# Kernel tuning notes

Hardware: AMD Instinct MI355X
Metric: run time of the kernel (lower is better)

Reference implementation:

```python
import jax, jax.numpy as jnp
import numpy as np

EMBED = 1024
HEADS = 16
HEAD_DIM = EMBED // HEADS


def setup_inputs() -> dict:
    key = jax.random.key(0)
    ks = jax.random.split(key, 7)
    N, S = 2, 2048
    k = jax.random.normal(ks[0], (N, S, EMBED), dtype=jnp.float32)
    q = jax.random.normal(ks[1], (N, S, EMBED), dtype=jnp.float32)
    v = jax.random.normal(ks[2], (N, S, EMBED), dtype=jnp.float32)
    sc = 1.0 / np.sqrt(HEAD_DIM)
    # nn.Linear weights, applied as x @ W.T
    Wk = jax.random.normal(ks[3], (HEAD_DIM, HEAD_DIM), dtype=jnp.float32) * sc
    Wq = jax.random.normal(ks[4], (HEAD_DIM, HEAD_DIM), dtype=jnp.float32) * sc
    Wv = jax.random.normal(ks[5], (HEAD_DIM, HEAD_DIM), dtype=jnp.float32) * sc
    Wo = jax.random.normal(ks[6], (EMBED, EMBED), dtype=jnp.float32) / np.sqrt(EMBED)
    return {"k": k, "q": q, "v": v, "Wk": Wk, "Wq": Wq, "Wv": Wv, "Wo": Wo}


def reference(k, q, v, Wk, Wq, Wv, Wo):
    N, S, _ = q.shape
    # reshape to [N, S, H, D]; per-head projection weights shared across heads
    kh = jnp.einsum('nshd,ed->nshe', k.reshape(N, S, HEADS, HEAD_DIM), Wk)
    qh = jnp.einsum('nshd,ed->nshe', q.reshape(N, S, HEADS, HEAD_DIM), Wq)
    vh = jnp.einsum('nshd,ed->nshe', v.reshape(N, S, HEADS, HEAD_DIM), Wv)
    # energy: [N, H, q_len, k_len]
    energy = jnp.einsum('nqhd,nkhd->nhqk', qh, kh)
    attn = jax.nn.softmax(energy / jnp.sqrt(jnp.float32(HEAD_DIM)), axis=-1)
    out = jnp.einsum('nhqk,nkhd->nqhd', attn, vh).reshape(N, S, EMBED)
    return out @ Wo.T
```

## Files before the change

kernel.cpp:

```cpp
#include <hip/hip_runtime.h>

#define SQ   2048
#define HEADS 16
#define HD   64
#define EMB  1024

typedef __attribute__((ext_vector_type(2))) __fp16 h2;
typedef __attribute__((ext_vector_type(4))) __fp16 h4;
typedef __attribute__((ext_vector_type(8))) __fp16 h8;
typedef __attribute__((ext_vector_type(4))) float f4;
typedef unsigned short USH;
typedef unsigned int   UI;

__device__ __forceinline__ UI pkh(float a, float b) {
    h2 v = __builtin_amdgcn_cvt_pkrtz(a, b);
    return __builtin_bit_cast(UI, v);
}

__device__ __forceinline__ void glds16(const void* g, void* l) {
    __builtin_amdgcn_global_load_lds(
        (const __attribute__((address_space(1))) unsigned int*)g,
        (__attribute__((address_space(3))) unsigned int*)l, 16, 0, 0);
}

__global__ __launch_bounds__(256) void proj_fused(
    const float* __restrict__ q_in, const float* __restrict__ k_in,
    const float* __restrict__ v_in, const float* __restrict__ Wq,
    const float* __restrict__ Wk,   const float* __restrict__ Wv,
    const float* __restrict__ Wo,
    USH* __restrict__ Qh, USH* __restrict__ Kh, USH* __restrict__ Vt,
    USH* __restrict__ Wob)
{
    int t = threadIdx.x;
    if (blockIdx.y == 3) {
        int i = blockIdx.x * 256 + t;
        for (int j = 0; j < 4; ++j) {
            float4 v = ((const float4*)Wo)[i + j * 65536];
            uint2 pk; pk.x = pkh(v.x, v.y); pk.y = pkh(v.z, v.w);
            *(uint2*)(Wob + ((size_t)i + (size_t)j * 65536) * 4) = pk;
        }
        return;
    }
    const float* X = (blockIdx.y == 0) ? q_in : (blockIdx.y == 1) ? k_in : v_in;
    const float* W = (blockIdx.y == 0) ? Wq   : (blockIdx.y == 1) ? Wk   : Wv;
    float scale    = (blockIdx.y == 0) ? 0.18033688011112043f : 1.0f;

    int bx = (blockIdx.x & 7) * 32 + (blockIdx.x >> 3);

    __shared__ __align__(16) USH Xl[256][72];
    __shared__ __align__(16) USH Wl[64][72];

    const float4* Xg = (const float4*)(X + (size_t)bx * 16384);
    for (int j = 0; j < 16; ++j) {
        int f = t + j * 256;
        float4 v = Xg[f];
        int row = f >> 4; int col = (f & 15) << 2;
        uint2 pk; pk.x = pkh(v.x, v.y); pk.y = pkh(v.z, v.w);
        *(uint2*)&Xl[row][col] = pk;
    }
    const float4* Wg = (const float4*)W;
    for (int j = 0; j < 4; ++j) {
        int f = t + j * 256;
        float4 v = Wg[f];
        int row = f >> 4; int col = (f & 15) << 2;
        uint2 pk; pk.x = pkh(v.x, v.y); pk.y = pkh(v.z, v.w);
        *(uint2*)&Wl[row][col] = pk;
    }
    __syncthreads();

    int wv = t >> 6, lane = t & 63, l4 = lane & 15, quad = lane >> 4;

    h8 wf[4][2], xf[4][2];
    for (int et = 0; et < 4; ++et)
        for (int ks = 0; ks < 2; ++ks)
            wf[et][ks] = *(const h8*)&Wl[et * 16 + l4][ks * 32 + quad * 8];
    for (int rt = 0; rt < 4; ++rt)
        for (int ks = 0; ks < 2; ++ks)
            xf[rt][ks] = *(const h8*)&Xl[wv * 64 + rt * 16 + l4][ks * 32 + quad * 8];

    f4 acc[4][4];
    for (int et = 0; et < 4; ++et)
        for (int rt = 0; rt < 4; ++rt) acc[et][rt] = (f4)(0.0f);
    for (int et = 0; et < 4; ++et)
        for (int rt = 0; rt < 4; ++rt)
            for (int ks = 0; ks < 2; ++ks)
                acc[et][rt] = __builtin_amdgcn_mfma_f32_16x16x32_f16(
                    wf[et][ks], xf[rt][ks], acc[et][rt], 0, 0, 0);

    if (blockIdx.y == 2) {
        int ns0 = bx * 16 + wv * 4;
        int n = ns0 >> 11, s = ns0 & 2047;
        for (int et = 0; et < 4; ++et)
            for (int j = 0; j < 4; ++j) {
                int e = et * 16 + quad * 4 + j;
                uint2 pk;
                pk.x = pkh(acc[et][0][j], acc[et][1][j]);
                pk.y = pkh(acc[et][2][j], acc[et][3][j]);
                *(uint2*)(Vt + (((size_t)(n * HEADS + l4) * HD + e) * SQ + s)) = pk;
            }
    } else {
        USH* Out = (blockIdx.y == 0) ? Qh : Kh;
        for (int rt = 0; rt < 4; ++rt) {
            int ns = bx * 16 + wv * 4 + rt;
            int n = ns >> 11, s = ns & 2047;
            USH* ob = Out + (((size_t)(n * HEADS) + l4) * SQ + s) * HD;
            for (int et = 0; et < 4; ++et) {
                uint2 pk;
                pk.x = pkh(acc[et][rt][0] * scale, acc[et][rt][1] * scale);
                pk.y = pkh(acc[et][rt][2] * scale, acc[et][rt][3] * scale);
                *(uint2*)(ob + et * 16 + quad * 4) = pk;
            }
        }
    }
}

__device__ __forceinline__ void stage_stripe(const USH* __restrict__ Kg,
                                             const USH* __restrict__ Vg,
                                             int kt, USH* wbuf,
                                             int w, int lane)
{
#pragma unroll
    for (int j = 0; j < 2; ++j) {
        int chunk = (lane >> 4) + j * 4;
        glds16(Kg + (size_t)(kt * 64 + w * 16 + (lane & 15)) * HD + chunk * 8,
               wbuf + j * 512);
    }
#pragma unroll
    for (int j = 0; j < 2; ++j) {
        int d = ((lane >> 5) + j * 2) * 16 + ((lane & 31) >> 1);
        glds16(Vg + (size_t)d * SQ + kt * 64 + w * 16 + (lane & 1) * 8,
               wbuf + 1024 + j * 512);
    }
}

__global__ __launch_bounds__(256, 3) void attn_kernel(
    const USH* __restrict__ Qh, const USH* __restrict__ Kh,
    const USH* __restrict__ Vt, USH* __restrict__ Oh)
{
    __shared__ union {
        USH wbuf[4][3][2048];
        struct { float Osum[64][68]; float Lsum[64]; } r;
    } lds;

    int t = threadIdx.x, w = t >> 6, lane = t & 63;
    int l4 = lane & 15, quad = lane >> 4;
    int b = blockIdx.x;
    int nh = b & 31;
    int q0 = (b >> 5) * 64;
    const USH* Qg = Qh + ((size_t)nh * SQ + q0) * HD;
    const USH* Kg = Kh + (size_t)nh * SQ * HD;
    const USH* Vg = Vt + (size_t)nh * HD * SQ;

    h8 bq[4][2];
#pragma unroll
    for (int qt = 0; qt < 4; ++qt)
#pragma unroll
        for (int ks = 0; ks < 2; ++ks)
            bq[qt][ks] = *(const h8*)(Qg + (size_t)(qt * 16 + l4) * HD + ks * 32 + quad * 8);

    f4 o[4][4];
#pragma unroll
    for (int dt = 0; dt < 4; ++dt)
#pragma unroll
        for (int qt = 0; qt < 4; ++qt) o[dt][qt] = (f4)(0.0f);
    float lsum[4] = {0.f, 0.f, 0.f, 0.f};

    int koff = quad * 128 + l4 * 8;
    int voff = 1024 + l4 * 16 + quad * 4;

    stage_stripe(Kg, Vg, 0, lds.wbuf[w][0], w, lane);
    stage_stripe(Kg, Vg, 1, lds.wbuf[w][1], w, lane);

    for (int i = 0; i < 16; ++i) {
        int tA = 2 * i, tB = 2 * i + 1;
        USH* bufA = lds.wbuf[w][tA % 3];
        USH* bufB = lds.wbuf[w][tB % 3];

        asm volatile("s_waitcnt vmcnt(0)" ::: "memory");
        __builtin_amdgcn_sched_barrier(0);

        h8 akA0 = *(const h8*)(bufA + koff);
        h8 akA1 = *(const h8*)(bufA + 512 + koff);
        h8 akB0 = *(const h8*)(bufB + koff);
        h8 akB1 = *(const h8*)(bufB + 512 + koff);
        h8 av8[4];
#pragma unroll
        for (int dt = 0; dt < 4; ++dt) {
            uint2 lo = *(const uint2*)(bufA + voff + dt * 256);
            uint2 hi = *(const uint2*)(bufB + voff + dt * 256);
            uint4 u; u.x = lo.x; u.y = lo.y; u.z = hi.x; u.w = hi.y;
            av8[dt] = __builtin_bit_cast(h8, u);
        }
        asm volatile("s_waitcnt lgkmcnt(0)" ::: "memory");
        __builtin_amdgcn_sched_barrier(0);
        if (i < 15) {
            stage_stripe(Kg, Vg, tA + 2, lds.wbuf[w][(tA + 2) % 3], w, lane);
            stage_stripe(Kg, Vg, tB + 2, lds.wbuf[w][(tB + 2) % 3], w, lane);
        }

        uint2 pA[4];
#pragma unroll
        for (int qt = 0; qt < 4; ++qt) {
            f4 s0 = __builtin_amdgcn_mfma_f32_16x16x32_f16(akA0, bq[qt][0], (f4)(0.0f), 0, 0, 0);
            f4 sc = __builtin_amdgcn_mfma_f32_16x16x32_f16(akA1, bq[qt][1], s0, 0, 0, 0);
            float p0 = __builtin_amdgcn_exp2f(sc[0]);
            float p1 = __builtin_amdgcn_exp2f(sc[1]);
            float p2 = __builtin_amdgcn_exp2f(sc[2]);
            float p3 = __builtin_amdgcn_exp2f(sc[3]);
            lsum[qt] += (p0 + p1) + (p2 + p3);
            pA[qt].x = pkh(p0, p1); pA[qt].y = pkh(p2, p3);
        }

#pragma unroll
        for (int qt = 0; qt < 4; ++qt) {
            f4 s0 = __builtin_amdgcn_mfma_f32_16x16x32_f16(akB0, bq[qt][0], (f4)(0.0f), 0, 0, 0);
            f4 sc = __builtin_amdgcn_mfma_f32_16x16x32_f16(akB1, bq[qt][1], s0, 0, 0, 0);
            float p0 = __builtin_amdgcn_exp2f(sc[0]);
            float p1 = __builtin_amdgcn_exp2f(sc[1]);
            float p2 = __builtin_amdgcn_exp2f(sc[2]);
            float p3 = __builtin_amdgcn_exp2f(sc[3]);
            lsum[qt] += (p0 + p1) + (p2 + p3);
            uint4 u;
            u.x = pA[qt].x; u.y = pA[qt].y;
            u.z = pkh(p0, p1); u.w = pkh(p2, p3);
            h8 pp = __builtin_bit_cast(h8, u);
#pragma unroll
            for (int dt = 0; dt < 4; ++dt)
                o[dt][qt] = __builtin_amdgcn_mfma_f32_16x16x32_f16(
                    av8[dt], pp, o[dt][qt], 0, 0, 0);
        }
    }

#pragma unroll
    for (int qt = 0; qt < 4; ++qt) {
        lsum[qt] += __shfl_xor(lsum[qt], 16, 64);
        lsum[qt] += __shfl_xor(lsum[qt], 32, 64);
    }

    __syncthreads();
    for (int ph = 0; ph < 4; ++ph) {
        if (w == ph) {
            for (int dt = 0; dt < 4; ++dt)
                for (int qt = 0; qt < 4; ++qt) {
                    float* dst = &lds.r.Osum[qt * 16 + l4][dt * 16 + quad * 4];
                    f4 val = o[dt][qt];
                    if (ph) val += *(const f4*)dst;
                    *(f4*)dst = val;
                }
            if (quad == 0)
                for (int qt = 0; qt < 4; ++qt) {
                    int qi = qt * 16 + l4;
                    lds.r.Lsum[qi] = ph ? (lds.r.Lsum[qi] + lsum[qt]) : lsum[qt];
                }
        }
        __syncthreads();
    }

    int n = nh >> 4, h = nh & 15;
    int q = t >> 2, d0 = (t & 3) * 16;
    float inv = 1.0f / lds.r.Lsum[q];
    float vv[16];
#pragma unroll
    for (int i = 0; i < 4; ++i) {
        f4 x = *(const f4*)&lds.r.Osum[q][d0 + i * 4];
        vv[i * 4 + 0] = x[0] * inv; vv[i * 4 + 1] = x[1] * inv;
        vv[i * 4 + 2] = x[2] * inv; vv[i * 4 + 3] = x[3] * inv;
    }
    uint4 ou0, ou1;
    ou0.x = pkh(vv[0], vv[1]);   ou0.y = pkh(vv[2], vv[3]);
    ou0.z = pkh(vv[4], vv[5]);   ou0.w = pkh(vv[6], vv[7]);
    ou1.x = pkh(vv[8], vv[9]);   ou1.y = pkh(vv[10], vv[11]);
    ou1.z = pkh(vv[12], vv[13]); ou1.w = pkh(vv[14], vv[15]);
    USH* ob = Oh + ((size_t)(n * SQ + q0 + q)) * EMB + h * HD + d0;
    *(uint4*)ob = ou0;
    *(uint4*)(ob + 8) = ou1;
}

__global__ __launch_bounds__(256, 4) void gemm_bt(const USH* __restrict__ A,
                                                  const USH* __restrict__ B,
                                                  float* __restrict__ C)
{
    __shared__ __align__(16) USH Al[2][4096];
    __shared__ __align__(16) USH Bl[2][4096];
    int t = threadIdx.x, w = t >> 6, lane = t & 63;
    int l4 = lane & 15, quad = lane >> 4;
    int b = blockIdx.x;
    int m0 = (b & 63) * 64;
    int n0 = (b >> 6) * 64;
    int wm = (w >> 1) * 32, wn = (w & 1) * 32;

    f4 acc[2][2];
    for (int mt = 0; mt < 2; ++mt)
        for (int nt = 0; nt < 2; ++nt) acc[mt][nt] = (f4)(0.0f);

    int aslot[2][2], bslot[2][2];
#pragma unroll
    for (int mt = 0; mt < 2; ++mt)
#pragma unroll
        for (int ks = 0; ks < 2; ++ks) {
            int m = wm + mt * 16 + l4;
            aslot[mt][ks] = m * 8 + ((ks * 4 + quad) ^ (m & 7));
            int nn = wn + mt * 16 + l4;
            bslot[mt][ks] = nn * 8 + ((ks * 4 + quad) ^ (nn & 7));
        }

#pragma unroll
    for (int j = 0; j < 2; ++j) {
        int s = (w * 2 + j) * 64 + lane;
        int r = s >> 3, c = (s & 7) ^ (r & 7);
        glds16(A + (size_t)(m0 + r) * 1024 + c * 8, Al[0] + s * 8);
        glds16(B + (size_t)(n0 + r) * 1024 + c * 8, Bl[0] + s * 8);
    }

    for (int ki = 0; ki < 16; ++ki) {
        int cur = ki & 1;
        __syncthreads();
        if (ki + 1 < 16) {
            int k0 = (ki + 1) * 64;
#pragma unroll
            for (int j = 0; j < 2; ++j) {
                int s = (w * 2 + j) * 64 + lane;
                int r = s >> 3, c = (s & 7) ^ (r & 7);
                glds16(A + (size_t)(m0 + r) * 1024 + k0 + c * 8, Al[cur ^ 1] + s * 8);
                glds16(B + (size_t)(n0 + r) * 1024 + k0 + c * 8, Bl[cur ^ 1] + s * 8);
            }
        }

        h8 a[2][2], bf[2][2];
#pragma unroll
        for (int mt = 0; mt < 2; ++mt)
#pragma unroll
            for (int ks = 0; ks < 2; ++ks) {
                a[mt][ks]  = *(const h8*)(Al[cur] + aslot[mt][ks] * 8);
                bf[mt][ks] = *(const h8*)(Bl[cur] + bslot[mt][ks] * 8);
            }
#pragma unroll
        for (int mt = 0; mt < 2; ++mt)
#pragma unroll
            for (int nt = 0; nt < 2; ++nt)
#pragma unroll
                for (int ks = 0; ks < 2; ++ks)
                    acc[mt][nt] = __builtin_amdgcn_mfma_f32_16x16x32_f16(
                        a[mt][ks], bf[nt][ks], acc[mt][nt], 0, 0, 0);
    }

    for (int mt = 0; mt < 2; ++mt)
        for (int nt = 0; nt < 2; ++nt)
            for (int r = 0; r < 4; ++r)
                C[(size_t)(m0 + wm + mt * 16 + quad * 4 + r) * 1024 +
                  (n0 + wn + nt * 16 + l4)] = acc[mt][nt][r];
}

extern "C" void kernel_launch(void* const* d_in, const int* in_sizes, int n_in,
                              void* d_out, int out_size, void* d_ws, size_t ws_size,
                              hipStream_t stream) {
    const float* k_in = (const float*)d_in[0];
    const float* q_in = (const float*)d_in[1];
    const float* v_in = (const float*)d_in[2];
    const float* Wk   = (const float*)d_in[3];
    const float* Wq   = (const float*)d_in[4];
    const float* Wv   = (const float*)d_in[5];
    const float* Wo   = (const float*)d_in[6];
    float* out = (float*)d_out;

    char* ws = (char*)d_ws;
    USH* Qh  = (USH*)(ws);
    USH* Kh  = (USH*)(ws + 8388608);
    USH* Vt  = (USH*)(ws + 16777216);
    USH* Oh  = (USH*)(ws + 25165824);
    USH* Wob = (USH*)(ws + 33554432);

    proj_fused<<<dim3(256, 4), dim3(256), 0, stream>>>(
        q_in, k_in, v_in, Wq, Wk, Wv, Wo, Qh, Kh, Vt, Wob);
    attn_kernel<<<dim3(1024), dim3(256), 0, stream>>>(Qh, Kh, Vt, Oh);
    gemm_bt<<<dim3(1024), dim3(256), 0, stream>>>(Oh, Wob, out);
}
```

Measured before the change: 182.5 us.

## Stage projection outputs through LDS for coalesced stores and enlarge output GEMM tile

The projection kernel now writes its MFMA results into a shared-memory union buffer, then emits 16-byte coalesced global stores for Q/K and the transposed V. Before, each lane wrote scattered 8-byte pieces. Separately, the output GEMM tile grows from 64x64 to 128x64, with four M sub-tiles per wave and a 512-block launch. This improves operand reuse but lowers occupancy (launch bounds 2) and leaves fewer blocks to fill the GPU.

After: 177.7 us. 2.6% less time.

```diff
diff --git a/kernel.cpp b/kernel.cpp
--- a/kernel.cpp
+++ b/kernel.cpp
@@ -47,8 +47,11 @@
 
     int bx = (blockIdx.x & 7) * 32 + (blockIdx.x >> 3);
 
-    __shared__ __align__(16) USH Xl[256][72];
-    __shared__ __align__(16) USH Wl[64][72];
+    __shared__ __align__(16) union {
+        struct { USH Xl[256][72]; USH Wl[64][72]; } in;
+        USH oqk[16 * 1160];
+        USH ov[16 * 1544];
+    } sm;
 
     const float4* Xg = (const float4*)(X + (size_t)bx * 16384);
     for (int j = 0; j < 16; ++j) {
@@ -56,7 +59,7 @@
         float4 v = Xg[f];
         int row = f >> 4; int col = (f & 15) << 2;
         uint2 pk; pk.x = pkh(v.x, v.y); pk.y = pkh(v.z, v.w);
-        *(uint2*)&Xl[row][col] = pk;
+        *(uint2*)&sm.in.Xl[row][col] = pk;
     }
     const float4* Wg = (const float4*)W;
     for (int j = 0; j < 4; ++j) {
@@ -64,7 +67,7 @@
         float4 v = Wg[f];
         int row = f >> 4; int col = (f & 15) << 2;
         uint2 pk; pk.x = pkh(v.x, v.y); pk.y = pkh(v.z, v.w);
-        *(uint2*)&Wl[row][col] = pk;
+        *(uint2*)&sm.in.Wl[row][col] = pk;
     }
     __syncthreads();
 
@@ -73,10 +76,12 @@
     h8 wf[4][2], xf[4][2];
     for (int et = 0; et < 4; ++et)
         for (int ks = 0; ks < 2; ++ks)
-            wf[et][ks] = *(const h8*)&Wl[et * 16 + l4][ks * 32 + quad * 8];
+            wf[et][ks] = *(const h8*)&sm.in.Wl[et * 16 + l4][ks * 32 + quad * 8];
     for (int rt = 0; rt < 4; ++rt)
         for (int ks = 0; ks < 2; ++ks)
-            xf[rt][ks] = *(const h8*)&Xl[wv * 64 + rt * 16 + l4][ks * 32 + quad * 8];
+            xf[rt][ks] = *(const h8*)&sm.in.Xl[wv * 64 + rt * 16 + l4][ks * 32 + quad * 8];
+
+    __syncthreads();
 
     f4 acc[4][4];
     for (int et = 0; et < 4; ++et)
@@ -87,29 +92,43 @@
                 acc[et][rt] = __builtin_amdgcn_mfma_f32_16x16x32_f16(
                     wf[et][ks], xf[rt][ks], acc[et][rt], 0, 0, 0);
 
+    int ns0 = bx * 16;
+    int n = ns0 >> 11, s0 = ns0 & 2047;
+
     if (blockIdx.y == 2) {
-        int ns0 = bx * 16 + wv * 4;
-        int n = ns0 >> 11, s = ns0 & 2047;
         for (int et = 0; et < 4; ++et)
             for (int j = 0; j < 4; ++j) {
                 int e = et * 16 + quad * 4 + j;
                 uint2 pk;
                 pk.x = pkh(acc[et][0][j], acc[et][1][j]);
                 pk.y = pkh(acc[et][2][j], acc[et][3][j]);
-                *(uint2*)(Vt + (((size_t)(n * HEADS + l4) * HD + e) * SQ + s)) = pk;
+                *(uint2*)&sm.ov[l4 * 1544 + e * 24 + wv * 4] = pk;
             }
+        __syncthreads();
+        for (int k = 0; k < 4; ++k) {
+            int g = k * 256 + t; int h = g >> 6, d = g & 63;
+            const USH* src = &sm.ov[h * 1544 + d * 24];
+            uint4 v0 = *(const uint4*)src;
+            uint4 v1 = *(const uint4*)(src + 8);
+            USH* dst = Vt + (((size_t)(n * HEADS + h) * HD + d) * SQ + s0);
+            *(uint4*)dst = v0;
+            *(uint4*)(dst + 8) = v1;
+        }
     } else {
         USH* Out = (blockIdx.y == 0) ? Qh : Kh;
-        for (int rt = 0; rt < 4; ++rt) {
-            int ns = bx * 16 + wv * 4 + rt;
-            int n = ns >> 11, s = ns & 2047;
-            USH* ob = Out + (((size_t)(n * HEADS) + l4) * SQ + s) * HD;
-            for (int et = 0; et < 4; ++et) {
+        for (int et = 0; et < 4; ++et)
+            for (int rt = 0; rt < 4; ++rt) {
                 uint2 pk;
                 pk.x = pkh(acc[et][rt][0] * scale, acc[et][rt][1] * scale);
                 pk.y = pkh(acc[et][rt][2] * scale, acc[et][rt][3] * scale);
-                *(uint2*)(ob + et * 16 + quad * 4) = pk;
+                *(uint2*)&sm.oqk[l4 * 1160 + (wv * 4 + rt) * 72 + et * 16 + quad * 4] = pk;
             }
+        __syncthreads();
+        for (int k = 0; k < 8; ++k) {
+            int g = k * 256 + t; int h = g >> 7, rem = g & 127;
+            int sl = rem >> 3, dq = (rem & 7) * 8;
+            uint4 v = *(const uint4*)&sm.oqk[h * 1160 + sl * 72 + dq];
+            *(uint4*)(Out + (((size_t)(n * HEADS + h) * SQ) + s0 + sl) * HD + dq) = v;
         }
     }
 }
@@ -276,39 +295,49 @@
     *(uint4*)(ob + 8) = ou1;
 }
 
-__global__ __launch_bounds__(256, 4) void gemm_bt(const USH* __restrict__ A,
+__global__ __launch_bounds__(256, 2) void gemm_bt(const USH* __restrict__ A,
                                                   const USH* __restrict__ B,
                                                   float* __restrict__ C)
 {
-    __shared__ __align__(16) USH Al[2][4096];
+    __shared__ __align__(16) USH Al[2][8192];
     __shared__ __align__(16) USH Bl[2][4096];
     int t = threadIdx.x, w = t >> 6, lane = t & 63;
     int l4 = lane & 15, quad = lane >> 4;
     int b = blockIdx.x;
-    int m0 = (b & 63) * 64;
-    int n0 = (b >> 6) * 64;
-    int wm = (w >> 1) * 32, wn = (w & 1) * 32;
-
-    f4 acc[2][2];
-    for (int mt = 0; mt < 2; ++mt)
+    int m0 = (b & 31) * 128;
+    int n0 = (b >> 5) * 64;
+    int wm = (w >> 1) * 64, wn = (w & 1) * 32;
+
+    f4 acc[4][2];
+    for (int mt = 0; mt < 4; ++mt)
         for (int nt = 0; nt < 2; ++nt) acc[mt][nt] = (f4)(0.0f);
 
-    int aslot[2][2], bslot[2][2];
-#pragma unroll
-    for (int mt = 0; mt < 2; ++mt)
+    int aslot[4][2], bslot[2][2];
+#pragma unroll
+    for (int mt = 0; mt < 4; ++mt)
 #pragma unroll
         for (int ks = 0; ks < 2; ++ks) {
             int m = wm + mt * 16 + l4;
             aslot[mt][ks] = m * 8 + ((ks * 4 + quad) ^ (m & 7));
-            int nn = wn + mt * 16 + l4;
-            bslot[mt][ks] = nn * 8 + ((ks * 4 + quad) ^ (nn & 7));
-        }
-
+        }
+#pragma unroll
+    for (int nt = 0; nt < 2; ++nt)
+#pragma unroll
+        for (int ks = 0; ks < 2; ++ks) {
+            int nn = wn + nt * 16 + l4;
+            bslot[nt][ks] = nn * 8 + ((ks * 4 + quad) ^ (nn & 7));
+        }
+
+#pragma unroll
+    for (int j = 0; j < 4; ++j) {
+        int s = (w * 4 + j) * 64 + lane;
+        int r = s >> 3, c = (s & 7) ^ (r & 7);
+        glds16(A + (size_t)(m0 + r) * 1024 + c * 8, Al[0] + s * 8);
+    }
 #pragma unroll
     for (int j = 0; j < 2; ++j) {
         int s = (w * 2 + j) * 64 + lane;
         int r = s >> 3, c = (s & 7) ^ (r & 7);
-        glds16(A + (size_t)(m0 + r) * 1024 + c * 8, Al[0] + s * 8);
         glds16(B + (size_t)(n0 + r) * 1024 + c * 8, Bl[0] + s * 8);
     }
 
@@ -318,24 +347,32 @@
         if (ki + 1 < 16) {
             int k0 = (ki + 1) * 64;
 #pragma unroll
+            for (int j = 0; j < 4; ++j) {
+                int s = (w * 4 + j) * 64 + lane;
+                int r = s >> 3, c = (s & 7) ^ (r & 7);
+                glds16(A + (size_t)(m0 + r) * 1024 + k0 + c * 8, Al[cur ^ 1] + s * 8);
+            }
+#pragma unroll
             for (int j = 0; j < 2; ++j) {
                 int s = (w * 2 + j) * 64 + lane;
                 int r = s >> 3, c = (s & 7) ^ (r & 7);
-                glds16(A + (size_t)(m0 + r) * 1024 + k0 + c * 8, Al[cur ^ 1] + s * 8);
                 glds16(B + (size_t)(n0 + r) * 1024 + k0 + c * 8, Bl[cur ^ 1] + s * 8);
             }
         }
 
-        h8 a[2][2], bf[2][2];
-#pragma unroll
-        for (int mt = 0; mt < 2; ++mt)
-#pragma unroll
-            for (int ks = 0; ks < 2; ++ks) {
-                a[mt][ks]  = *(const h8*)(Al[cur] + aslot[mt][ks] * 8);
-                bf[mt][ks] = *(const h8*)(Bl[cur] + bslot[mt][ks] * 8);
-            }
-#pragma unroll
-        for (int mt = 0; mt < 2; ++mt)
+        h8 a[4][2], bf[2][2];
+#pragma unroll
+        for (int mt = 0; mt < 4; ++mt)
+#pragma unroll
+            for (int ks = 0; ks < 2; ++ks)
+                a[mt][ks] = *(const h8*)(Al[cur] + aslot[mt][ks] * 8);
+#pragma unroll
+        for (int nt = 0; nt < 2; ++nt)
+#pragma unroll
+            for (int ks = 0; ks < 2; ++ks)
+                bf[nt][ks] = *(const h8*)(Bl[cur] + bslot[nt][ks] * 8);
+#pragma unroll
+        for (int mt = 0; mt < 4; ++mt)
 #pragma unroll
             for (int nt = 0; nt < 2; ++nt)
 #pragma unroll
@@ -344,7 +381,7 @@
                         a[mt][ks], bf[nt][ks], acc[mt][nt], 0, 0, 0);
     }
 
-    for (int mt = 0; mt < 2; ++mt)
+    for (int mt = 0; mt < 4; ++mt)
         for (int nt = 0; nt < 2; ++nt)
             for (int r = 0; r < 4; ++r)
                 C[(size_t)(m0 + wm + mt * 16 + quad * 4 + r) * 1024 +
@@ -373,5 +410,5 @@
     proj_fused<<<dim3(256, 4), dim3(256), 0, stream>>>(
         q_in, k_in, v_in, Wq, Wk, Wv, Wo, Qh, Kh, Vt, Wob);
     attn_kernel<<<dim3(1024), dim3(256), 0, stream>>>(Qh, Kh, Vt, Oh);
-    gemm_bt<<<dim3(1024), dim3(256), 0, stream>>>(Oh, Wob, out);
-}
+    gemm_bt<<<dim3(512), dim3(256), 0, stream>>>(Oh, Wob, out);
+}
```
